# Performance work log

Measured on AMD Instinct MI355X. Metric: run time of the kernel, lower is better.

The kernel has to match this reference:

```python
import jax, jax.numpy as jnp
import numpy as np

NUM_HEADS = 8
NUM_LEVELS = 4
NUM_POINTS = 8
SPATIAL_SHAPES = np.array([[92, 160], [46, 80], [23, 40], [12, 20]], dtype=np.int64)


def _bilinear_sample(val_hw, loc, Hl, Wl):
    """val_hw: (bs, heads, H*W, d); loc: (bs, nq, heads, P, 2) in [0,1].
    Matches torch grid_sample(bilinear, zeros padding, align_corners=False)
    applied to grid = 2*loc - 1, i.e. pixel coords x = loc_x*W - 0.5.
    Returns (bs, heads, nq, P, d)."""
    x = loc[..., 0] * Wl - 0.5
    y = loc[..., 1] * Hl - 0.5
    x0 = jnp.floor(x)
    y0 = jnp.floor(y)
    wx = (x - x0).transpose(0, 2, 1, 3)  # (bs, heads, nq, P)
    wy = (y - y0).transpose(0, 2, 1, 3)
    x0i = x0.astype(jnp.int32).transpose(0, 2, 1, 3)
    y0i = y0.astype(jnp.int32).transpose(0, 2, 1, 3)

    def gather(ix, iy):
        valid = ((ix >= 0) & (ix < Wl) & (iy >= 0) & (iy < Hl)).astype(val_hw.dtype)
        idx = jnp.clip(iy, 0, Hl - 1) * Wl + jnp.clip(ix, 0, Wl - 1)  # (bs,heads,nq,P)
        b, h, nq, P = idx.shape
        g = jnp.take_along_axis(val_hw, idx.reshape(b, h, nq * P, 1), axis=2)
        return g.reshape(b, h, nq, P, -1) * valid[..., None]

    return (gather(x0i, y0i) * ((1 - wx) * (1 - wy))[..., None]
            + gather(x0i + 1, y0i) * (wx * (1 - wy))[..., None]
            + gather(x0i, y0i + 1) * ((1 - wx) * wy)[..., None]
            + gather(x0i + 1, y0i + 1) * (wx * wy)[..., None])


def setup_inputs() -> dict:
    key = jax.random.key(0)
    ks = jax.random.split(key, 10)
    C = 256
    bs, nq = 2, 10000
    nv = int((SPATIAL_SHAPES[:, 0] * SPATIAL_SHAPES[:, 1]).sum())  # 19560
    s = 1.0 / np.sqrt(C)
    return {
        "query": jax.random.normal(ks[0], (bs, nq, C), dtype=jnp.float32),
        "value": jax.random.normal(ks[1], (bs, nv, C), dtype=jnp.float32),
        "reference_points": jax.random.uniform(ks[2], (bs, nq, 4, 2), dtype=jnp.float32),
        "spatial_shapes": SPATIAL_SHAPES,
        "W_value": jax.random.normal(ks[3], (C, C), dtype=jnp.float32) * s,
        "b_value": jnp.zeros((C,), dtype=jnp.float32),
        "W_off": jax.random.normal(ks[4], (C, NUM_HEADS * NUM_LEVELS * NUM_POINTS * 2), dtype=jnp.float32) * 0.01,
        "b_off": jax.random.normal(ks[5], (NUM_HEADS * NUM_LEVELS * NUM_POINTS * 2,), dtype=jnp.float32) * 0.1,
        "W_attn": jax.random.normal(ks[6], (C, NUM_HEADS * NUM_LEVELS * NUM_POINTS), dtype=jnp.float32) * s,
        "b_attn": jnp.zeros((NUM_HEADS * NUM_LEVELS * NUM_POINTS,), dtype=jnp.float32),
    }


def reference(query, value, reference_points, spatial_shapes,
              W_value, b_value, W_off, b_off, W_attn, b_attn):
    bs, nq, C = query.shape
    NH, NL, NP = NUM_HEADS, NUM_LEVELS, NUM_POINTS
    d = C // NH
    Z = reference_points.shape[2]  # num_Z_anchors
    shapes_np = np.asarray(spatial_shapes)  # static host-side shapes

    # value / offset / attention projections
    v = (value @ W_value + b_value).reshape(bs, -1, NH, d)
    off = (query @ W_off + b_off).reshape(bs, nq, NH, NL, NP, 2)
    attn = jax.nn.softmax((query @ W_attn + b_attn).reshape(bs, nq, NH, NL * NP), axis=-1)
    attn = attn.reshape(bs, nq, NH, NL, NP)

    # normalize offsets by (W, H) per level and add to reference points
    norm = jnp.stack([spatial_shapes[:, 1], spatial_shapes[:, 0]], -1).astype(query.dtype)  # (NL, 2)
    off = off / norm[None, None, None, :, None, :]
    off = off.reshape(bs, nq, NH, NL, NP // Z, Z, 2)
    loc = reference_points[:, :, None, None, None, :, :] + off  # (bs,nq,NH,NL,NP//Z,Z,2)
    loc = loc.reshape(bs, nq, NH, NL, NP, 2)

    out = jnp.zeros((bs, NH, nq, d), dtype=query.dtype)
    start = 0
    for l in range(NL):
        Hl, Wl = int(shapes_np[l, 0]), int(shapes_np[l, 1])
        v_l = v[:, start:start + Hl * Wl].transpose(0, 2, 1, 3)  # (bs, NH, H*W, d)
        start += Hl * Wl
        sampled = _bilinear_sample(v_l, loc[:, :, :, l], Hl, Wl)  # (bs,NH,nq,NP,d)
        out = out + jnp.einsum('bhqpd,bqhp->bhqd', sampled, attn[:, :, :, l])
    return out.transpose(0, 2, 1, 3).reshape(bs, nq, NH * d)
```

## Files before the change

### kernel.cpp

```cpp
#include <hip/hip_runtime.h>
#include <math.h>

#define NH 8
#define NL 4
#define NP 8
#define CDIM 256
#define NQ 10000
#define BS 2
#define NV 19560

__constant__ int LVL_H[NL]     = {92, 46, 23, 12};
__constant__ int LVL_W[NL]     = {160, 80, 40, 20};
__constant__ int LVL_START[NL] = {0, 14720, 18400, 19320};

typedef __attribute__((ext_vector_type(8))) short short8;
typedef __attribute__((ext_vector_type(4))) float f32x4;
typedef __attribute__((ext_vector_type(8))) _Float16 half8;

__device__ __forceinline__ unsigned short f2bf(float f) {
    unsigned int u = __float_as_uint(f);
    u += 0x7fffu + ((u >> 16) & 1u);
    return (unsigned short)(u >> 16);
}

__global__ __launch_bounds__(256) void cvt_bf16(
    const float* __restrict__ src, unsigned short* __restrict__ dst, int n4)
{
    const int i = blockIdx.x * 256 + threadIdx.x;
    if (i >= n4) return;
    const float4 f = ((const float4*)src)[i];
    ushort4 o;
    o.x = f2bf(f.x); o.y = f2bf(f.y); o.z = f2bf(f.z); o.w = f2bf(f.w);
    ((ushort4*)dst)[i] = o;
}

__global__ __launch_bounds__(256) void prep_weights(
    const float* __restrict__ Wv,
    const float* __restrict__ Woff, const float* __restrict__ boff,
    const float* __restrict__ Wattn, const float* __restrict__ battn,
    unsigned short* __restrict__ BvalT, unsigned short* __restrict__ BcatT,
    float* __restrict__ biascat)
{
    const int n = blockIdx.x;
    const int t = threadIdx.x;
    if (n < 256) {
        BvalT[n * 256 + t] = f2bf(Wv[t * 256 + n]);
    } else if (n < 1024) {
        const int m = n - 256;
        const float v = (m < 512) ? Woff[t * 512 + m] : Wattn[t * 256 + (m - 512)];
        BcatT[m * 256 + t] = f2bf(v);
    } else {
        #pragma unroll
        for (int s = 0; s < 3; s++) {
            const int i = s * 256 + t;
            biascat[i] = (i < 512) ? boff[i] : battn[i - 512];
        }
    }
}

#define AST 130
template <int MODE>
__global__ __launch_bounds__(256) void gemm_bias_mfma(
    const unsigned short* __restrict__ A, const unsigned short* __restrict__ Bt,
    const float* __restrict__ bias, _Float16* __restrict__ Ch, int M, int N)
{
    __shared__ short8 Al[4 * AST];
    __shared__ short8 Bl[4 * AST];

    const int t = threadIdx.x;
    const int rowBase = blockIdx.x * 128;
    const int colBase = blockIdx.y * 128;

    const int w  = t >> 6;
    const int l  = t & 63;
    const int wm = (w >> 1) * 64;
    const int wn = (w & 1) * 64;
    const int row16 = l & 15;
    const int kg    = l >> 4;

    const int sr = t >> 1;
    const int sh = t & 1;

    f32x4 acc[4][4] = {};

    for (int k0 = 0; k0 < 256; k0 += 32) {
        {
            const int grow = rowBase + sr;
            short8 v0 = {}, v1 = {};
            if (grow < M) {
                const unsigned short* ap = A + (size_t)grow * 256 + k0 + sh * 16;
                v0 = *(const short8*)ap;
                v1 = *(const short8*)(ap + 8);
            }
            Al[(sh * 2 + 0) * AST + sr] = v0;
            Al[(sh * 2 + 1) * AST + sr] = v1;
        }
        {
            const unsigned short* bp = Bt + (size_t)(colBase + sr) * 256 + k0 + sh * 16;
            Bl[(sh * 2 + 0) * AST + sr] = *(const short8*)bp;
            Bl[(sh * 2 + 1) * AST + sr] = *(const short8*)(bp + 8);
        }
        __syncthreads();

        short8 af[4], bfr[4];
        #pragma unroll
        for (int i = 0; i < 4; i++) af[i] = Al[kg * AST + wm + i * 16 + row16];
        #pragma unroll
        for (int j = 0; j < 4; j++) bfr[j] = Bl[kg * AST + wn + j * 16 + row16];
        #pragma unroll
        for (int i = 0; i < 4; i++)
            #pragma unroll
            for (int j = 0; j < 4; j++)
                acc[i][j] = __builtin_amdgcn_mfma_f32_16x16x32_bf16(
                    af[i], bfr[j], acc[i][j], 0, 0, 0);
        __syncthreads();
    }

    const int crow0 = rowBase + wm + (l >> 4) * 4;
    const int ccol0 = colBase + wn + (l & 15);
    float bv[4];
    #pragma unroll
    for (int j = 0; j < 4; j++) bv[j] = bias[ccol0 + j * 16];
    #pragma unroll
    for (int i = 0; i < 4; i++) {
        #pragma unroll
        for (int r = 0; r < 4; r++) {
            const int row = crow0 + i * 16 + r;
            if (row >= M) continue;
            #pragma unroll
            for (int j = 0; j < 4; j++) {
                const float val = acc[i][j][r] + bv[j];
                const int col = ccol0 + j * 16;
                if (MODE == 0) {
                    Ch[(size_t)row * N + col] = (_Float16)val;
                } else {
                    const int b   = row / NV;
                    const int pix = row - b * NV;
                    const int h   = col >> 5;
                    const int ch  = col & 31;
                    Ch[((size_t)(b * NH + h) * NV + pix) * 32 + ch] = (_Float16)val;
                }
            }
        }
    }
}

__global__ __launch_bounds__(256) void sample_kernel(
    const _Float16* __restrict__ vproj,
    const _Float16* __restrict__ offcat,
    const float* __restrict__ refpts,
    float* __restrict__ out)
{
    const int bid = blockIdx.x;
    const int h   = bid & 7;
    const int g   = bid >> 3;
    const int b   = g & 1;
    const int q0  = (g >> 1) * 8;
    const int t   = threadIdx.x;

    __shared__ float4 desc[8 * 64];

    const int qi = t >> 5, j = t & 31;
    const int qrow = b * NQ + q0 + qi;

    {
        const int lv = j >> 3, p = j & 7;

        float logit = (float)offcat[(size_t)qrow * 768 + 512 + h * 32 + j];
        float m = logit;
        #pragma unroll
        for (int s = 16; s > 0; s >>= 1) m = fmaxf(m, __shfl_xor(m, s, 32));
        float e = __expf(logit - m);
        float ssum = e;
        #pragma unroll
        for (int s = 16; s > 0; s >>= 1) ssum += __shfl_xor(ssum, s, 32);
        const float aw = e / ssum;

        const int Wl = LVL_W[lv], Hl = LVL_H[lv], st = LVL_START[lv];
        const float offx = (float)offcat[(size_t)qrow * 768 + h * 64 + j * 2];
        const float offy = (float)offcat[(size_t)qrow * 768 + h * 64 + j * 2 + 1];

        const int z = p & 3;
        const float rx = refpts[((size_t)qrow * 4 + z) * 2];
        const float ry = refpts[((size_t)qrow * 4 + z) * 2 + 1];

        const float x = fmaf(rx, (float)Wl, offx) - 0.5f;
        const float y = fmaf(ry, (float)Hl, offy) - 0.5f;
        const float x0f = floorf(x), y0f = floorf(y);
        const float wx = x - x0f, wy = y - y0f;
        const int x0 = (int)x0f, y0 = (int)y0f;

        const int xb = min(max(x0, 0), Wl - 2);
        const float wl = (x0 >= 0 && x0 < Wl)          ? (1.f - wx) : 0.f;
        const float wr = (x0 + 1 >= 0 && x0 + 1 < Wl)  ? wx         : 0.f;
        const float wA = (x0 == xb) ? wl : ((x0 + 1 == xb) ? wr : 0.f);
        const float wB = (x0 == xb) ? wr : ((x0 == xb + 1) ? wl : 0.f);

        #pragma unroll
        for (int r = 0; r < 2; r++) {
            const int yy = y0 + r;
            const float rwv = (yy >= 0 && yy < Hl)
                            ? (r ? wy : (1.f - wy)) * aw : 0.f;
            const int iy = min(max(yy, 0), Hl - 1);
            float4 d;
            d.x = __int_as_float(st + iy * Wl + xb);
            d.y = wA * rwv;
            d.z = wB * rwv;
            d.w = 0.f;
            desc[qi * 64 + j * 2 + r] = d;
        }
    }
    __syncthreads();

    const int lane = t & 31;
    const int grp  = lane >> 3;
    const int sub  = lane & 7;
    const int pix  = sub >> 2;
    const int chq  = sub & 3;

    const _Float16* slab = vproj + (size_t)(b * NH + h) * NV * 32;
    const float4* dq = &desc[qi * 64];

    float acc[8] = {};
    #pragma unroll 4
    for (int i = 0; i < 16; i++) {
        const float4 dsc = dq[i * 4 + grp];
        const int   lidx = __float_as_int(dsc.x);
        const float w    = pix ? dsc.z : dsc.y;
        const half8 v = *(const half8*)(slab + (size_t)(lidx + pix) * 32 + chq * 8);
        #pragma unroll
        for (int e = 0; e < 8; e++)
            acc[e] += w * (float)v[e];
    }

    #pragma unroll
    for (int s = 4; s <= 16; s <<= 1)
        #pragma unroll
        for (int e = 0; e < 8; e++) acc[e] += __shfl_xor(acc[e], s, 32);

    if ((lane & 0x1C) == 0) {
        float* op = out + (size_t)qrow * 256 + h * 32 + chq * 8;
        *(float4*)op       = make_float4(acc[0], acc[1], acc[2], acc[3]);
        *(float4*)(op + 4) = make_float4(acc[4], acc[5], acc[6], acc[7]);
    }
}

extern "C" void kernel_launch(void* const* d_in, const int* in_sizes, int n_in,
                              void* d_out, int out_size, void* d_ws, size_t ws_size,
                              hipStream_t stream)
{
    const float* query   = (const float*)d_in[0];
    const float* value   = (const float*)d_in[1];
    const float* refpts  = (const float*)d_in[2];
    const float* W_value = (const float*)d_in[4];
    const float* b_value = (const float*)d_in[5];
    const float* W_off   = (const float*)d_in[6];
    const float* b_off   = (const float*)d_in[7];
    const float* W_attn  = (const float*)d_in[8];
    const float* b_attn  = (const float*)d_in[9];

    char* ws = (char*)d_ws;
    _Float16*       vproj   = (_Float16*)(ws);
    unsigned short* valuebf = (unsigned short*)(ws + 20029440);
    unsigned short* querybf = (unsigned short*)(ws + 40058880);
    _Float16*       offcat  = (_Float16*)(ws + 50298880);
    unsigned short* BvalT   = (unsigned short*)(ws + 81018880);
    unsigned short* BcatT   = (unsigned short*)(ws + 81149952);
    float*          biascat = (float*)(ws + 81543168);

    const dim3 blk(256);

    cvt_bf16<<<dim3(9780), blk, 0, stream>>>(value, valuebf, BS * NV * 256 / 4);
    cvt_bf16<<<dim3(5000), blk, 0, stream>>>(query, querybf, BS * NQ * 256 / 4);
    prep_weights<<<dim3(1025), blk, 0, stream>>>(W_value, W_off, b_off,
                                                 W_attn, b_attn,
                                                 BvalT, BcatT, biascat);

    gemm_bias_mfma<1><<<dim3((BS * NV + 127) / 128, 2), blk, 0, stream>>>(
        valuebf, BvalT, b_value, vproj, BS * NV, CDIM);

    gemm_bias_mfma<0><<<dim3((BS * NQ + 127) / 128, 6), blk, 0, stream>>>(
        querybf, BcatT, biascat, offcat, BS * NQ, 768);

    sample_kernel<<<dim3(BS * NQ), blk, 0, stream>>>(
        vproj, offcat, refpts, (float*)d_out);
}
```

Measured before the change: 225.0 us.

## Merge prep and GEMM launches, vectorize GEMM stores, use packed fp16 sampling accumulation

The three conversion and weight-prep kernels become one launch, and the two projection GEMMs become one launch that picks its operands by block index. Launch overhead and tail gaps between kernels should shrink. The MFMA operands are swapped so each lane holds four consecutive columns, which allows half4 vector stores and float4 bias loads in the epilogue. The sampling loop now accumulates in packed fp16 half2 FMAs instead of fp32, cutting conversion and ALU work at the cost of lower accumulation precision.

```diff
diff --git a/kernel.cpp b/kernel.cpp
--- a/kernel.cpp
+++ b/kernel.cpp
@@ -15,7 +15,8 @@
 
 typedef __attribute__((ext_vector_type(8))) short short8;
 typedef __attribute__((ext_vector_type(4))) float f32x4;
-typedef __attribute__((ext_vector_type(8))) _Float16 half8;
+typedef __attribute__((ext_vector_type(2))) _Float16 half2v;
+typedef __attribute__((ext_vector_type(4))) _Float16 half4v;
 
 __device__ __forceinline__ unsigned short f2bf(float f) {
     unsigned int u = __float_as_uint(f);
@@ -23,54 +24,79 @@
     return (unsigned short)(u >> 16);
 }
 
-__global__ __launch_bounds__(256) void cvt_bf16(
-    const float* __restrict__ src, unsigned short* __restrict__ dst, int n4)
-{
-    const int i = blockIdx.x * 256 + threadIdx.x;
-    if (i >= n4) return;
-    const float4 f = ((const float4*)src)[i];
-    ushort4 o;
-    o.x = f2bf(f.x); o.y = f2bf(f.y); o.z = f2bf(f.z); o.w = f2bf(f.w);
-    ((ushort4*)dst)[i] = o;
-}
-
-__global__ __launch_bounds__(256) void prep_weights(
+__global__ __launch_bounds__(256) void prep_all(
+    const float* __restrict__ value, const float* __restrict__ query,
     const float* __restrict__ Wv,
     const float* __restrict__ Woff, const float* __restrict__ boff,
     const float* __restrict__ Wattn, const float* __restrict__ battn,
+    unsigned short* __restrict__ valuebf, unsigned short* __restrict__ querybf,
     unsigned short* __restrict__ BvalT, unsigned short* __restrict__ BcatT,
     float* __restrict__ biascat)
 {
-    const int n = blockIdx.x;
-    const int t = threadIdx.x;
-    if (n < 256) {
-        BvalT[n * 256 + t] = f2bf(Wv[t * 256 + n]);
-    } else if (n < 1024) {
-        const int m = n - 256;
-        const float v = (m < 512) ? Woff[t * 512 + m] : Wattn[t * 256 + (m - 512)];
-        BcatT[m * 256 + t] = f2bf(v);
+    const int bid = blockIdx.x;
+    const int t   = threadIdx.x;
+    if (bid < 9780) {
+        const int i = bid * 256 + t;
+        const float4 f = ((const float4*)value)[i];
+        ushort4 o;
+        o.x = f2bf(f.x); o.y = f2bf(f.y); o.z = f2bf(f.z); o.w = f2bf(f.w);
+        ((ushort4*)valuebf)[i] = o;
+    } else if (bid < 14780) {
+        const int i = (bid - 9780) * 256 + t;
+        const float4 f = ((const float4*)query)[i];
+        ushort4 o;
+        o.x = f2bf(f.x); o.y = f2bf(f.y); o.z = f2bf(f.z); o.w = f2bf(f.w);
+        ((ushort4*)querybf)[i] = o;
     } else {
-        #pragma unroll
-        for (int s = 0; s < 3; s++) {
-            const int i = s * 256 + t;
-            biascat[i] = (i < 512) ? boff[i] : battn[i - 512];
+        const int n = bid - 14780;
+        if (n < 256) {
+            BvalT[n * 256 + t] = f2bf(Wv[t * 256 + n]);
+        } else if (n < 1024) {
+            const int m = n - 256;
+            const float v = (m < 512) ? Woff[t * 512 + m]
+                                      : Wattn[t * 256 + (m - 512)];
+            BcatT[m * 256 + t] = f2bf(v);
+        } else {
+            #pragma unroll
+            for (int s = 0; s < 3; s++) {
+                const int i = s * 256 + t;
+                biascat[i] = (i < 512) ? boff[i] : battn[i - 512];
+            }
         }
     }
 }
 
 #define AST 130
-template <int MODE>
-__global__ __launch_bounds__(256) void gemm_bias_mfma(
-    const unsigned short* __restrict__ A, const unsigned short* __restrict__ Bt,
-    const float* __restrict__ bias, _Float16* __restrict__ Ch, int M, int N)
+__global__ __launch_bounds__(256) void gemm_all(
+    const unsigned short* __restrict__ valuebf,
+    const unsigned short* __restrict__ BvalT,
+    const float* __restrict__ b_value, _Float16* __restrict__ vproj,
+    const unsigned short* __restrict__ querybf,
+    const unsigned short* __restrict__ BcatT,
+    const float* __restrict__ biascat, _Float16* __restrict__ offcat)
 {
     __shared__ short8 Al[4 * AST];
     __shared__ short8 Bl[4 * AST];
 
+    const int bid = blockIdx.x;
+    const bool modeV = bid < 612;
+
+    const unsigned short* A;
+    const unsigned short* Bt;
+    const float* bias;
+    int M, N, rowBase, colBase;
+    if (modeV) {
+        A = valuebf; Bt = BvalT; bias = b_value;
+        M = BS * NV; N = 256;
+        rowBase = (bid >> 1) * 128; colBase = (bid & 1) * 128;
+    } else {
+        const int b2 = bid - 612;
+        A = querybf; Bt = BcatT; bias = biascat;
+        M = BS * NQ; N = 768;
+        rowBase = (b2 / 6) * 128; colBase = (b2 % 6) * 128;
+    }
+
     const int t = threadIdx.x;
-    const int rowBase = blockIdx.x * 128;
-    const int colBase = blockIdx.y * 128;
-
     const int w  = t >> 6;
     const int l  = t & 63;
     const int wm = (w >> 1) * 64;
@@ -112,35 +138,36 @@
             #pragma unroll
             for (int j = 0; j < 4; j++)
                 acc[i][j] = __builtin_amdgcn_mfma_f32_16x16x32_bf16(
-                    af[i], bfr[j], acc[i][j], 0, 0, 0);
+                    bfr[j], af[i], acc[i][j], 0, 0, 0);
         __syncthreads();
     }
 
-    const int crow0 = rowBase + wm + (l >> 4) * 4;
-    const int ccol0 = colBase + wn + (l & 15);
-    float bv[4];
-    #pragma unroll
-    for (int j = 0; j < 4; j++) bv[j] = bias[ccol0 + j * 16];
+    const int m16 = l & 15;
+    const int q4  = (l >> 4) * 4;
     #pragma unroll
     for (int i = 0; i < 4; i++) {
-        #pragma unroll
-        for (int r = 0; r < 4; r++) {
-            const int row = crow0 + i * 16 + r;
-            if (row >= M) continue;
-            #pragma unroll
-            for (int j = 0; j < 4; j++) {
-                const float val = acc[i][j][r] + bv[j];
-                const int col = ccol0 + j * 16;
-                if (MODE == 0) {
-                    Ch[(size_t)row * N + col] = (_Float16)val;
-                } else {
-                    const int b   = row / NV;
-                    const int pix = row - b * NV;
-                    const int h   = col >> 5;
-                    const int ch  = col & 31;
-                    Ch[((size_t)(b * NH + h) * NV + pix) * 32 + ch] = (_Float16)val;
-                }
+        const int row = rowBase + wm + i * 16 + m16;
+        if (row >= M) continue;
+        #pragma unroll
+        for (int j = 0; j < 4; j++) {
+            const int col0 = colBase + wn + j * 16 + q4;
+            const float4 bv = *(const float4*)&bias[col0];
+            half4v o;
+            o[0] = (_Float16)(acc[i][j][0] + bv.x);
+            o[1] = (_Float16)(acc[i][j][1] + bv.y);
+            o[2] = (_Float16)(acc[i][j][2] + bv.z);
+            o[3] = (_Float16)(acc[i][j][3] + bv.w);
+            _Float16* dst;
+            if (modeV) {
+                const int b   = (row >= NV) ? 1 : 0;
+                const int pix = row - b * NV;
+                const int h   = col0 >> 5;
+                const int ch  = col0 & 31;
+                dst = vproj + ((size_t)(b * NH + h) * NV + pix) * 32 + ch;
+            } else {
+                dst = offcat + (size_t)row * 768 + col0;
             }
+            *(half4v*)dst = o;
         }
     }
 }
@@ -218,30 +245,35 @@
     const int pix  = sub >> 2;
     const int chq  = sub & 3;
 
-    const _Float16* slab = vproj + (size_t)(b * NH + h) * NV * 32;
+    const _Float16* slab = vproj + (size_t)(b * NH + h) * NV * 32 + chq * 8;
     const float4* dq = &desc[qi * 64];
 
-    float acc[8] = {};
-    #pragma unroll 4
+    half2v a0 = {}, a1 = {}, a2 = {}, a3 = {};
+    #pragma unroll 8
     for (int i = 0; i < 16; i++) {
         const float4 dsc = dq[i * 4 + grp];
         const int   lidx = __float_as_int(dsc.x);
         const float w    = pix ? dsc.z : dsc.y;
-        const half8 v = *(const half8*)(slab + (size_t)(lidx + pix) * 32 + chq * 8);
-        #pragma unroll
-        for (int e = 0; e < 8; e++)
-            acc[e] += w * (float)v[e];
-    }
-
+        const _Float16 wh = (_Float16)w;
+        half2v wv; wv[0] = wh; wv[1] = wh;
+        const uint4 u = *(const uint4*)(slab + (size_t)(lidx + pix) * 32);
+        a0 += wv * __builtin_bit_cast(half2v, u.x);
+        a1 += wv * __builtin_bit_cast(half2v, u.y);
+        a2 += wv * __builtin_bit_cast(half2v, u.z);
+        a3 += wv * __builtin_bit_cast(half2v, u.w);
+    }
+
+    float accf[8] = {(float)a0[0], (float)a0[1], (float)a1[0], (float)a1[1],
+                     (float)a2[0], (float)a2[1], (float)a3[0], (float)a3[1]};
     #pragma unroll
     for (int s = 4; s <= 16; s <<= 1)
         #pragma unroll
-        for (int e = 0; e < 8; e++) acc[e] += __shfl_xor(acc[e], s, 32);
+        for (int e = 0; e < 8; e++) accf[e] += __shfl_xor(accf[e], s, 32);
 
     if ((lane & 0x1C) == 0) {
         float* op = out + (size_t)qrow * 256 + h * 32 + chq * 8;
-        *(float4*)op       = make_float4(acc[0], acc[1], acc[2], acc[3]);
-        *(float4*)(op + 4) = make_float4(acc[4], acc[5], acc[6], acc[7]);
+        *(float4*)op       = make_float4(accf[0], accf[1], accf[2], accf[3]);
+        *(float4*)(op + 4) = make_float4(accf[4], accf[5], accf[6], accf[7]);
     }
 }
 
@@ -270,17 +302,13 @@
 
     const dim3 blk(256);
 
-    cvt_bf16<<<dim3(9780), blk, 0, stream>>>(value, valuebf, BS * NV * 256 / 4);
-    cvt_bf16<<<dim3(5000), blk, 0, stream>>>(query, querybf, BS * NQ * 256 / 4);
-    prep_weights<<<dim3(1025), blk, 0, stream>>>(W_value, W_off, b_off,
-                                                 W_attn, b_attn,
-                                                 BvalT, BcatT, biascat);
-
-    gemm_bias_mfma<1><<<dim3((BS * NV + 127) / 128, 2), blk, 0, stream>>>(
-        valuebf, BvalT, b_value, vproj, BS * NV, CDIM);
-
-    gemm_bias_mfma<0><<<dim3((BS * NQ + 127) / 128, 6), blk, 0, stream>>>(
-        querybf, BcatT, biascat, offcat, BS * NQ, 768);
+    prep_all<<<dim3(15805), blk, 0, stream>>>(
+        value, query, W_value, W_off, b_off, W_attn, b_attn,
+        valuebf, querybf, BvalT, BcatT, biascat);
+
+    gemm_all<<<dim3(1554), blk, 0, stream>>>(
+        valuebf, BvalT, b_value, vproj,
+        querybf, BcatT, biascat, offcat);
 
     sample_kernel<<<dim3(BS * NQ), blk, 0, stream>>>(
         vproj, offcat, refpts, (float*)d_out);
```

New measurement: 214.9 us. 1.05x faster.
